# Optimization experiments

Hardware: AMD Instinct MI355X
Metric: run time of the kernel (lower is better)

Reference implementation:

```python
import jax, jax.numpy as jnp
import numpy as np
from jax import lax

V, E, HE, HD, B, T, DEC_STEPS = 50000, 300, 512, 1024, 64, 400, 80


def gru_cell(x, h, w_ih, w_hh, b_ih, b_hh):
    # PyTorch GRU cell semantics
    gi = x @ w_ih.T + b_ih          # [B, 3H]
    gh = h @ w_hh.T + b_hh          # [B, 3H]
    ir, iz, in_ = jnp.split(gi, 3, axis=-1)
    hr, hz, hn = jnp.split(gh, 3, axis=-1)
    r = jax.nn.sigmoid(ir + hr)
    z = jax.nn.sigmoid(iz + hz)
    n = jnp.tanh(in_ + r * hn)
    return (1.0 - z) * n + z * h


def setup_inputs() -> dict:
    key = jax.random.key(0)
    ks = jax.random.split(key, 20)
    s = 0.05
    texts = jax.random.randint(ks[0], (B, T), 0, V, dtype=jnp.int32)
    text_length = jax.random.randint(ks[1], (B,), 1, T + 1, dtype=jnp.int32)
    emb = jax.random.normal(ks[2], (V, E), jnp.float32) * s
    def w(k, shape):
        return jax.random.normal(k, shape, jnp.float32) * s
    return {
        "texts": texts,
        "text_length": text_length,
        "emb": emb,
        "enc_wih_f": w(ks[3], (3 * HE, E)),
        "enc_whh_f": w(ks[4], (3 * HE, HE)),
        "enc_bih_f": w(ks[5], (3 * HE,)),
        "enc_bhh_f": w(ks[6], (3 * HE,)),
        "enc_wih_b": w(ks[7], (3 * HE, E)),
        "enc_whh_b": w(ks[8], (3 * HE, HE)),
        "enc_bih_b": w(ks[9], (3 * HE,)),
        "enc_bhh_b": w(ks[10], (3 * HE,)),
        "dec_wih": w(ks[11], (3 * HD, E)),
        "dec_whh": w(ks[12], (3 * HD, HD)),
        "dec_bih": w(ks[13], (3 * HD,)),
        "dec_bhh": w(ks[14], (3 * HD,)),
        "out_w": w(ks[15], (V, HD)),
        "out_b": w(ks[16], (V,)),
    }


def reference(texts, text_length, emb,
              enc_wih_f, enc_whh_f, enc_bih_f, enc_bhh_f,
              enc_wih_b, enc_whh_b, enc_bih_b, enc_bhh_b,
              dec_wih, dec_whh, dec_bih, dec_bhh,
              out_w, out_b):
    b, t = texts.shape
    embed = emb[texts]                      # [B,T,E] (dropout is identity in eval)
    xs = jnp.swapaxes(embed, 0, 1)          # [T,B,E]
    lens = text_length[:, None]             # [B,1]
    h0 = jnp.zeros((b, HE), emb.dtype)

    # forward direction: final hidden = state at last valid timestep (pack semantics)
    def fstep(h, inp):
        x, tt = inp
        hn = gru_cell(x, h, enc_wih_f, enc_whh_f, enc_bih_f, enc_bhh_f)
        return jnp.where(tt < lens, hn, h), None
    hf, _ = lax.scan(fstep, h0, (xs, jnp.arange(t)))

    # backward direction: processes x[len-1] ... x[0]; skip padded positions
    def bstep(h, inp):
        x, tt = inp
        hn = gru_cell(x, h, enc_wih_b, enc_whh_b, enc_bih_b, enc_bhh_b)
        return jnp.where(tt < lens, hn, h), None
    hb, _ = lax.scan(bstep, h0, (xs[::-1], jnp.arange(t)[::-1]))

    hidden = jnp.concatenate([hf, hb], axis=-1)   # [B, 1024]

    sos = jnp.ones((b,), jnp.int32)               # inputs = ones
    def dstep(carry, _):
        h, tok = carry
        x = emb[tok]                              # [B,E]
        h = gru_cell(x, h, dec_wih, dec_whh, dec_bih, dec_bhh)
        logits = h @ out_w.T + out_b              # [B,V]
        tok = jnp.argmax(logits, axis=-1).astype(jnp.int32)
        return (h, tok), tok
    _, toks = lax.scan(dstep, (hidden, sos), None, length=DEC_STEPS)  # [80,B]

    return jnp.swapaxes(toks, 0, 1).astype(jnp.float32)[:, :, None]  # [B,80,1]
```

## Files before the change

### kernel.cpp

```cpp
#include <hip/hip_runtime.h>
#include <stdint.h>

typedef unsigned int u32;
typedef unsigned long long u64;
typedef unsigned short u16;
typedef __attribute__((ext_vector_type(8))) short s8;
typedef __attribute__((ext_vector_type(4))) float f4;

#define NWG 256
#define TPB 512
#define NB 64
#define TT 400
#define EE 300
#define HEN 512
#define HD 1024
#define VV 50000
#define DEC 80
#define NTL 3125
#define NTLP 3136
#define LCAP 512
#define PBOFF 131072
#define SMEMSZ (PBOFF + 16384)
#define RESC 0.00837f

#define BD_GRP   0
#define BD_ROOT  1024
#define BD_EPO   1152
#define BF_GRP   1280
#define BF_ROOT  2304
#define BF_EPO   2368
#define BX_GRP   2432
#define BX_ROOT  3456
#define BX_EPO   3520
#define BAR_WORDS 3584

struct P {
  const int* texts; const int* len; const float* emb;
  const float* ewih0; const float* ewhh0; const float* ebih0; const float* ebhh0;
  const float* ewih1; const float* ewhh1; const float* ebih1; const float* ebhh1;
  const float* dwih; const float* dwhh; const float* dbih; const float* dbhh;
  const float* outw; const float* outb;
  float* out;
  u16* owbf; float* xT; float* hTf; float* hTb; float* hTd; u16* hbf;
  u64* prt; int* tok; float* wn;
  u32* bar;
};

__device__ __forceinline__ float cld(const float* a) {
  return __hip_atomic_load(const_cast<float*>(a), __ATOMIC_RELAXED, __HIP_MEMORY_SCOPE_AGENT);
}
__device__ __forceinline__ void cst(float* a, float v) {
  __hip_atomic_store(a, v, __ATOMIC_RELAXED, __HIP_MEMORY_SCOPE_AGENT);
}
__device__ __forceinline__ u64 cld(const u64* a) {
  return __hip_atomic_load(const_cast<u64*>(a), __ATOMIC_RELAXED, __HIP_MEMORY_SCOPE_AGENT);
}
__device__ __forceinline__ void cst(u64* a, u64 v) {
  __hip_atomic_store(a, v, __ATOMIC_RELAXED, __HIP_MEMORY_SCOPE_AGENT);
}
__device__ __forceinline__ int cld(const int* a) {
  return __hip_atomic_load(const_cast<int*>(a), __ATOMIC_RELAXED, __HIP_MEMORY_SCOPE_AGENT);
}
__device__ __forceinline__ void cst(int* a, int v) {
  __hip_atomic_store(a, v, __ATOMIC_RELAXED, __HIP_MEMORY_SCOPE_AGENT);
}
__device__ __forceinline__ void cst(u16* a, u16 v) {
  __hip_atomic_store(a, v, __ATOMIC_RELAXED, __HIP_MEMORY_SCOPE_AGENT);
}

__device__ __forceinline__ void gbarx(u32* grp, u32* root, u32* epo,
                                      u32 e, u32 gsz, u32 nroot) {
  __syncthreads();
  if (threadIdx.x == 0) {
    u32 old = __hip_atomic_fetch_add(grp, 1u, __ATOMIC_RELAXED, __HIP_MEMORY_SCOPE_AGENT);
    if (old == e * gsz + (gsz - 1u)) {
      u32 r = __hip_atomic_fetch_add(root, 1u, __ATOMIC_RELAXED, __HIP_MEMORY_SCOPE_AGENT);
      if (r == e * nroot + (nroot - 1u))
        __hip_atomic_store(epo, e + 1u, __ATOMIC_RELAXED, __HIP_MEMORY_SCOPE_AGENT);
    }
    while (__hip_atomic_load(epo, __ATOMIC_RELAXED, __HIP_MEMORY_SCOPE_AGENT) < e + 1u)
      __builtin_amdgcn_s_sleep(8);
  }
  __syncthreads();
}

__device__ __forceinline__ u32 fkey(float v) {
  u32 u = __float_as_uint(v);
  return (u & 0x80000000u) ? ~u : (u | 0x80000000u);
}
__device__ __forceinline__ u16 f2bf(float f) {
  u32 u = __float_as_uint(f);
  u32 r = u + 0x7FFFu + ((u >> 16) & 1u);
  return (u16)(r >> 16);
}
__device__ __forceinline__ float sigm(float x) { return 1.f / (1.f + expf(-x)); }

__device__ __forceinline__ void gru_combine_epi(
    char* smem, const f4& ar, const f4& az, const f4& ax, const f4& ah,
    int jjb, int HL, const float* bih, const float* bhh,
    const float* hc, float* ho, int mask_t, const int* lenp, u16* hbf_out)
{
  const int tid = threadIdx.x, lane = tid & 63, wv = tid >> 6;
  float* pb = (float*)(smem + PBOFF);
  const int wl = wv & 3;
  if (wv < 4) {
    #pragma unroll
    for (int j = 0; j < 4; j++) {
      pb[((wl * 16 + j * 4 + 0) * 64) + lane] = ar[j];
      pb[((wl * 16 + j * 4 + 1) * 64) + lane] = az[j];
      pb[((wl * 16 + j * 4 + 2) * 64) + lane] = ax[j];
      pb[((wl * 16 + j * 4 + 3) * 64) + lane] = ah[j];
    }
  }
  __syncthreads();
  if (wv >= 4) {
    #pragma unroll
    for (int j = 0; j < 4; j++) {
      pb[((wl * 16 + j * 4 + 0) * 64) + lane] += ar[j];
      pb[((wl * 16 + j * 4 + 1) * 64) + lane] += az[j];
      pb[((wl * 16 + j * 4 + 2) * 64) + lane] += ax[j];
      pb[((wl * 16 + j * 4 + 3) * 64) + lane] += ah[j];
    }
  }
  __syncthreads();
  if (tid < 256) {
    int b = tid & 63, j = tid >> 6;
    int jj = jjb + j;
    float r = 0, z = 0, xn = 0, hn = 0;
    #pragma unroll
    for (int w = 0; w < 4; w++) {
      int base = ((w * 16 + j * 4) * 64) + b;
      r  += pb[base];
      z  += pb[base + 64];
      xn += pb[base + 128];
      hn += pb[base + 192];
    }
    r = sigm(r + bih[jj] + bhh[jj]);
    z = sigm(z + bih[HL + jj] + bhh[HL + jj]);
    float nn = tanhf(xn + bih[2 * HL + jj] + r * (hn + bhh[2 * HL + jj]));
    float hold = cld(hc + (size_t)jj * NB + b);
    float hv = (1.f - z) * nn + z * hold;
    if (lenp && mask_t >= lenp[b]) hv = hold;
    cst(ho + (size_t)jj * NB + b, hv);
    if (hbf_out) cst(hbf_out + (size_t)b * HD + jj, f2bf(hv));
  }
}

__device__ __forceinline__ void gru_enc(
    char* smem, int jjb, const float* xsrc,
    const float* bih, const float* bhh,
    const float* __restrict__ hc, float* ho, int tt, const int* lenp)
{
  const int tid = threadIdx.x, lane = tid & 63, wv = tid >> 6;
  const float* lw = (const float*)smem;
  const int KT = EE + HEN;
  const int vs = (wv * KT) >> 3, ve = ((wv + 1) * KT) >> 3;
  f4 ar = {0,0,0,0}, az = {0,0,0,0}, ax = {0,0,0,0}, ah = {0,0,0,0};
  const int xe = ve < EE ? ve : EE;
  int k = vs;
  for (; k + 8 <= xe; k += 8) {
    float xv[8];
    #pragma unroll
    for (int u = 0; u < 8; u++) xv[u] = xsrc[(size_t)(k + u) * NB + lane];
    #pragma unroll
    for (int u = 0; u < 8; u++) {
      const float* wp = lw + (k + u) * 12;
      f4 w0 = *(const f4*)wp; f4 w1 = *(const f4*)(wp + 4); f4 w2 = *(const f4*)(wp + 8);
      ar += xv[u] * w0; az += xv[u] * w1; ax += xv[u] * w2;
    }
  }
  for (; k < xe; k++) {
    float xv = xsrc[(size_t)k * NB + lane];
    const float* wp = lw + k * 12;
    f4 w0 = *(const f4*)wp; f4 w1 = *(const f4*)(wp + 4); f4 w2 = *(const f4*)(wp + 8);
    ar += xv * w0; az += xv * w1; ax += xv * w2;
  }
  k = vs > EE ? vs : EE;
  for (; k + 8 <= ve; k += 8) {
    float hv[8];
    #pragma unroll
    for (int u = 0; u < 8; u++) hv[u] = cld(hc + (size_t)(k + u - EE) * NB + lane);
    #pragma unroll
    for (int u = 0; u < 8; u++) {
      const float* wp = lw + (k + u) * 12;
      f4 w0 = *(const f4*)wp; f4 w1 = *(const f4*)(wp + 4); f4 w2 = *(const f4*)(wp + 8);
      ar += hv[u] * w0; az += hv[u] * w1; ah += hv[u] * w2;
    }
  }
  for (; k < ve; k++) {
    float hv = cld(hc + (size_t)(k - EE) * NB + lane);
    const float* wp = lw + k * 12;
    f4 w0 = *(const f4*)wp; f4 w1 = *(const f4*)(wp + 4); f4 w2 = *(const f4*)(wp + 8);
    ar += hv * w0; az += hv * w1; ah += hv * w2;
  }
  gru_combine_epi(smem, ar, az, ax, ah, jjb, HEN, bih, bhh, hc, ho, tt, lenp, nullptr);
}

__device__ __forceinline__ void gru_dec(
    const P& p, char* smem, int jjb,
    const float* __restrict__ hc, float* ho)
{
  const int tid = threadIdx.x, lane = tid & 63, wv = tid >> 6;
  const float* wih = p.dwih; const float* whh = p.dwhh;
  const int KT = EE + HD;
  const int vs = (wv * KT) >> 3, ve = ((wv + 1) * KT) >> 3;
  f4 ar = {0,0,0,0}, az = {0,0,0,0}, ax = {0,0,0,0}, ah = {0,0,0,0};
  const int xe = ve < EE ? ve : EE;
  if (vs < EE) {
    const float* xr = p.emb + (size_t)cld(p.tok + lane) * EE;
    int k = vs;
    for (; k + 4 <= xe; k += 4) {
      float xv[4];
      #pragma unroll
      for (int u = 0; u < 4; u++) xv[u] = xr[k + u];
      #pragma unroll
      for (int u = 0; u < 4; u++) {
        #pragma unroll
        for (int j = 0; j < 4; j++) {
          int jj = jjb + j;
          ar[j] = fmaf(xv[u], wih[(size_t)jj * EE + k + u], ar[j]);
          az[j] = fmaf(xv[u], wih[(size_t)(HD + jj) * EE + k + u], az[j]);
          ax[j] = fmaf(xv[u], wih[(size_t)(2 * HD + jj) * EE + k + u], ax[j]);
        }
      }
    }
    for (; k < xe; k++) {
      float xv = xr[k];
      #pragma unroll
      for (int j = 0; j < 4; j++) {
        int jj = jjb + j;
        ar[j] = fmaf(xv, wih[(size_t)jj * EE + k], ar[j]);
        az[j] = fmaf(xv, wih[(size_t)(HD + jj) * EE + k], az[j]);
        ax[j] = fmaf(xv, wih[(size_t)(2 * HD + jj) * EE + k], ax[j]);
      }
    }
  }
  int hs = vs - EE; if (hs < 0) hs = 0;
  const int he = ve - EE;
  int k = hs;
  for (; k + 4 <= he; k += 4) {
    float hv[4];
    #pragma unroll
    for (int u = 0; u < 4; u++) hv[u] = cld(hc + (size_t)(k + u) * NB + lane);
    #pragma unroll
    for (int u = 0; u < 4; u++) {
      #pragma unroll
      for (int j = 0; j < 4; j++) {
        int jj = jjb + j;
        ar[j] = fmaf(hv[u], whh[(size_t)jj * HD + k + u], ar[j]);
        az[j] = fmaf(hv[u], whh[(size_t)(HD + jj) * HD + k + u], az[j]);
        ah[j] = fmaf(hv[u], whh[(size_t)(2 * HD + jj) * HD + k + u], ah[j]);
      }
    }
  }
  for (; k < he; k++) {
    float hv = cld(hc + (size_t)k * NB + lane);
    #pragma unroll
    for (int j = 0; j < 4; j++) {
      int jj = jjb + j;
      ar[j] = fmaf(hv, whh[(size_t)jj * HD + k], ar[j]);
      az[j] = fmaf(hv, whh[(size_t)(HD + jj) * HD + k], az[j]);
      ah[j] = fmaf(hv, whh[(size_t)(2 * HD + jj) * HD + k], ah[j]);
    }
  }
  gru_combine_epi(smem, ar, az, ax, ah, jjb, HD, p.dbih, p.dbhh,
                  hc, ho, -1, nullptr, p.hbf);
}

__global__ void __launch_bounds__(TPB, 2) prep_kernel(P p) {
  const int wg = blockIdx.x, tid = threadIdx.x;
  const int lane = tid & 63, wv = tid >> 6;
  const int gtid = wg * TPB + tid;
  int gwv = wg * 8 + wv;
  for (int v = gwv; v < VV; v += 2048) {
    const float* wr = p.outw + (size_t)v * HD + lane * 16;
    u16* dst = p.owbf + (size_t)v * HD + lane * 16;
    float sa = 0.f;
    u32 pk[8];
    #pragma unroll
    for (int q = 0; q < 4; q++) {
      float4 f = *(const float4*)(wr + q * 4);
      sa += f.x * f.x + f.y * f.y + f.z * f.z + f.w * f.w;
      pk[q * 2 + 0] = (u32)f2bf(f.x) | ((u32)f2bf(f.y) << 16);
      pk[q * 2 + 1] = (u32)f2bf(f.z) | ((u32)f2bf(f.w) << 16);
    }
    *(uint4*)(dst)     = make_uint4(pk[0], pk[1], pk[2], pk[3]);
    *(uint4*)(dst + 8) = make_uint4(pk[4], pk[5], pk[6], pk[7]);
    #pragma unroll
    for (int d = 1; d < 64; d <<= 1) sa += __shfl_xor(sa, d);
    if (lane == 0) p.wn[v] = sqrtf(sa);
  }
  const long long tot = (long long)TT * NB * EE;
  for (long long i = gtid; i < tot; i += (long long)NWG * TPB) {
    int t = (int)(i / (NB * EE));
    int rr = (int)(i % (NB * EE));
    int b2 = rr / EE, k = rr % EE;
    float v = p.emb[(size_t)p.texts[b2 * TT + t] * EE + k];
    p.xT[((size_t)t * EE + k) * NB + b2] = v;
  }
}

__global__ void __launch_bounds__(TPB, 1) enc_kernel(P p) {
  extern __shared__ __align__(16) char smem[];
  const int wg = blockIdx.x, tid = threadIdx.x;
  const int lane = tid & 63, wv = tid >> 6;
  const int gtid = wg * TPB + tid;
  u32 ebD = 0, ebF = 0;
  const int dir = wg >> 7;
  const int ejjb = (wg & 127) * 4;

  {
    const float* wih = dir ? p.ewih1 : p.ewih0;
    const float* whh = dir ? p.ewhh1 : p.ewhh0;
    float* lw = (float*)smem;
    for (int c = wv; c < 12; c += 8) {
      int g = c >> 2, j = c & 3;
      const float* sx = wih + (size_t)(g * HEN + ejjb + j) * EE;
      for (int k = lane; k < EE; k += 64) lw[k * 12 + c] = sx[k];
      const float* sh = whh + (size_t)(g * HEN + ejjb + j) * HEN;
      for (int k = lane; k < HEN; k += 64) lw[(EE + k) * 12 + c] = sh[k];
    }
  }
  __syncthreads();

  {
    const float* bih = dir ? p.ebih1 : p.ebih0;
    const float* bhh = dir ? p.ebhh1 : p.ebhh0;
    float* hbase = dir ? p.hTb : p.hTf;
    for (int t = 0; t < TT; t++) {
      int te = dir ? (TT - 1 - t) : t;
      const float* hc = hbase + (size_t)(t & 1) * HEN * NB;
      float* ho = hbase + (size_t)((t + 1) & 1) * HEN * NB;
      gru_enc(smem, ejjb, p.xT + (size_t)te * EE * NB, bih, bhh, hc, ho, te, p.len);
      gbarx(p.bar + BD_GRP + ((wg >> 4) << 6),
            p.bar + BD_ROOT + dir * 64, p.bar + BD_EPO + dir * 64, ebD++, 16u, 8u);
    }
  }
  gbarx(p.bar + BF_GRP + ((wg >> 4) << 6),
        p.bar + BF_ROOT, p.bar + BF_EPO, ebF++, 16u, 16u);
  for (int i = gtid; i < HD * NB; i += NWG * TPB) {
    int k = i / NB, b2 = i % NB;
    float v = (k < HEN) ? cld(p.hTf + (size_t)k * NB + b2)
                        : cld(p.hTb + (size_t)(k - HEN) * NB + b2);
    cst(p.hTd + i, v);
  }
  if (gtid < NB) cst(p.tok + gtid, 1);
}

__global__ void __launch_bounds__(TPB, 1) dec_kernel(P p) {
  extern __shared__ __align__(16) char smem[];
  const int wg = blockIdx.x, tid = threadIdx.x;
  const int lane = tid & 63, wv = tid >> 6;
  u32 ebX = 0;

  for (int s = 0; s < DEC; s++) {
    const float* hc = p.hTd + (size_t)(s & 1) * HD * NB;
    float* ho = p.hTd + (size_t)((s + 1) & 1) * HD * NB;
    gru_dec(p, smem, wg * 4, hc, ho);
    gbarx(p.bar + BX_GRP + ((wg >> 4) << 6),
          p.bar + BX_ROOT, p.bar + BX_EPO, ebX++, 16u, 16u);
    {
      u16* hA = (u16*)smem;
      float* hsq = (float*)(smem + PBOFF);
      const int l15 = lane & 15, quad = lane >> 4;
      const int gw = wg * 8 + wv;
      const bool two = (gw + 2048) < NTL;
      if (tid < 64) hsq[tid] = 0.f;
      __syncthreads();
      const u64* hb64 = (const u64*)p.hbf;
      u64* hA64 = (u64*)hA;
      #pragma unroll 1
      for (int ii = 0; ii < 32; ii += 4) {
        u64 q[4];
        #pragma unroll
        for (int u = 0; u < 4; u++)
          q[u] = cld(hb64 + (size_t)(tid + (ii + u) * TPB));
        #pragma unroll
        for (int u = 0; u < 4; u++) {
          int i = tid + (ii + u) * TPB;
          int r = i >> 8, c = i & 255;
          int cc = c >> 1;
          hA64[(size_t)r * 256 + ((cc ^ (r & 7)) * 2) + (c & 1)] = q[u];
          u32 uu[2] = {(u32)q[u], (u32)(q[u] >> 32)};
          float sq = 0.f;
          #pragma unroll
          for (int t2 = 0; t2 < 2; t2++) {
            float lo = __uint_as_float(uu[t2] << 16);
            float hi = __uint_as_float(uu[t2] & 0xffff0000u);
            sq = fmaf(lo, lo, fmaf(hi, hi, sq));
          }
          atomicAdd(&hsq[r], sq);
        }
      }
      __syncthreads();
      f4 acc0[4], acc1[4];
      #pragma unroll
      for (int m = 0; m < 4; m++) {
        #pragma unroll
        for (int r = 0; r < 4; r++) { acc0[m][r] = 0.f; acc1[m][r] = 0.f; }
      }
      const u16* bp0 = p.owbf + (size_t)(gw * 16 + l15) * HD + quad * 8;
      const u16* bp1 = bp0 + (size_t)2048 * 16 * HD;
      const int x7 = l15 & 7;
      const u16* hrow = hA + l15 * 1024;
      #pragma unroll 4
      for (int kc = 0; kc < 32; kc++) {
        int ci = ((kc * 4 + quad) ^ x7) * 8;
        s8 b0 = *(const s8*)(bp0 + kc * 32);
        s8 a0 = *(const s8*)(hrow + ci);
        s8 a1 = *(const s8*)(hrow + 16384 + ci);
        s8 a2 = *(const s8*)(hrow + 32768 + ci);
        s8 a3 = *(const s8*)(hrow + 49152 + ci);
        acc0[0] = __builtin_amdgcn_mfma_f32_16x16x32_bf16(a0, b0, acc0[0], 0, 0, 0);
        acc0[1] = __builtin_amdgcn_mfma_f32_16x16x32_bf16(a1, b0, acc0[1], 0, 0, 0);
        acc0[2] = __builtin_amdgcn_mfma_f32_16x16x32_bf16(a2, b0, acc0[2], 0, 0, 0);
        acc0[3] = __builtin_amdgcn_mfma_f32_16x16x32_bf16(a3, b0, acc0[3], 0, 0, 0);
        if (two) {
          s8 b1 = *(const s8*)(bp1 + kc * 32);
          acc1[0] = __builtin_amdgcn_mfma_f32_16x16x32_bf16(a0, b1, acc1[0], 0, 0, 0);
          acc1[1] = __builtin_amdgcn_mfma_f32_16x16x32_bf16(a1, b1, acc1[1], 0, 0, 0);
          acc1[2] = __builtin_amdgcn_mfma_f32_16x16x32_bf16(a2, b1, acc1[2], 0, 0, 0);
          acc1[3] = __builtin_amdgcn_mfma_f32_16x16x32_bf16(a3, b1, acc1[3], 0, 0, 0);
        }
      }
      float hroot[4][4];
      #pragma unroll
      for (int m = 0; m < 4; m++)
        #pragma unroll
        for (int r = 0; r < 4; r++)
          hroot[m][r] = sqrtf(hsq[m * 16 + quad * 4 + r]);
      auto epi = [&](int nt, f4* acc) {
        int col = nt * 16 + l15;
        float bias = p.outb[col];
        float wnc = p.wn[col];
        #pragma unroll
        for (int m = 0; m < 4; m++) {
          #pragma unroll
          for (int r = 0; r < 4; r++) {
            float v = acc[m][r] + bias;
            float e = RESC * hroot[m][r] * wnc + 1e-5f;
            u32 klo = fkey(v - e), kup = fkey(v + e);
            #pragma unroll
            for (int d = 1; d < 16; d <<= 1) {
              u32 ol = __shfl_xor(klo, d); if (ol > klo) klo = ol;
              u32 ou = __shfl_xor(kup, d); if (ou > kup) kup = ou;
            }
            if (l15 == 0)
              cst(p.prt + (size_t)(m * 16 + quad * 4 + r) * NTLP + nt,
                  ((u64)klo << 32) | kup);
          }
        }
      };
      epi(gw, acc0);
      if (two) epi(gw + 2048, acc1);
    }
    gbarx(p.bar + BX_GRP + ((wg >> 4) << 6),
          p.bar + BX_ROOT, p.bar + BX_EPO, ebX++, 16u, 16u);
    if (wg < NB) {
      const int b = wg;
      char* ms = smem + PBOFF;
      float* hb = (float*)ms;
      u64* red = (u64*)(ms + 4096);
      u64* gmp = (u64*)(ms + 4160);
      u64* bestp = (u64*)(ms + 4168);
      int* ncp = (int*)(ms + 4176);
      int* list = (int*)(ms + 4192);
      for (int i = tid; i < HD; i += TPB) hb[i] = cld(ho + (size_t)i * NB + b);
      if (tid == 0) { *bestp = 0ull; *ncp = 0; }
      __syncthreads();
      u64 pv[7];
      u64 mx = 0;
      #pragma unroll
      for (int i = 0; i < 7; i++) {
        int nt = tid + i * TPB;
        pv[i] = (nt < NTL) ? cld(p.prt + (size_t)b * NTLP + nt) : 0ull;
        if (pv[i] > mx) mx = pv[i];
      }
      #pragma unroll
      for (int d = 1; d < 64; d <<= 1) { u64 o = __shfl_xor(mx, d); if (o > mx) mx = o; }
      if (lane == 0) red[wv] = mx;
      __syncthreads();
      if (tid == 0) {
        u64 g = red[0];
        for (int w2 = 1; w2 < 8; w2++) if (red[w2] > g) g = red[w2];
        *gmp = g;
      }
      __syncthreads();
      const u32 thr = (u32)(*gmp >> 32);
      #pragma unroll
      for (int i = 0; i < 7; i++) {
        if ((u32)pv[i] >= thr) {
          int ix = atomicAdd(ncp, 1);
          if (ix < LCAP) list[ix] = tid + i * TPB;
        }
      }
      __syncthreads();
      int total = *ncp;
      int nc = total < LCAP ? total : LCAP;
      const int c16 = tid >> 5, seg = tid & 31;
      u64 lb = 0;
      auto rescue = [&](int nt) {
        int v = nt * 16 + c16;
        const float* wr = p.outw + (size_t)v * HD;
        float sm = 0.f;
        #pragma unroll 8
        for (int i = 0; i < 32; i++) {
          int k = seg + 32 * i;
          sm = fmaf(hb[k], wr[k], sm);
        }
        #pragma unroll
        for (int d = 1; d < 32; d <<= 1) sm += __shfl_xor(sm, d);
        if (seg == 0) {
          float lg = sm + p.outb[v];
          u64 k2 = ((u64)fkey(lg) << 32) | (~(u32)v);
          if (k2 > lb) lb = k2;
        }
      };
      for (int ci = 0; ci < nc; ci++) rescue(list[ci]);
      if (total > LCAP) {
        for (int nt = 0; nt < NTL; nt++)
          if ((u32)cld(p.prt + (size_t)b * NTLP + nt) >= thr) rescue(nt);
      }
      if (seg == 0 && lb) atomicMax((unsigned long long*)bestp, lb);
      __syncthreads();
      if (tid == 0) {
        u32 v = ~(u32)(*bestp);
        cst(p.tok + b, (int)v);
        p.out[b * DEC + s] = (float)v;
      }
    }
    gbarx(p.bar + BX_GRP + ((wg >> 4) << 6),
          p.bar + BX_ROOT, p.bar + BX_EPO, ebX++, 16u, 16u);
  }
}

__global__ void seq2seq_init(u32* bar, float* hTf, float* hTb) {
  int g = blockIdx.x * blockDim.x + threadIdx.x;
  if (g < BAR_WORDS) bar[g] = 0u;
  int n = 2 * HEN * NB;
  for (int i = g; i < n; i += gridDim.x * blockDim.x) { hTf[i] = 0.f; hTb[i] = 0.f; }
}

extern "C" void kernel_launch(void* const* d_in, const int* in_sizes, int n_in,
                              void* d_out, int out_size, void* d_ws, size_t ws_size,
                              hipStream_t stream) {
  char* w = (char*)d_ws;
  size_t off = 0;
  auto carve = [&](size_t n) {
    void* q = w + off;
    off = (off + n + 255) & ~(size_t)255;
    return q;
  };
  P p;
  p.texts = (const int*)d_in[0];
  p.len   = (const int*)d_in[1];
  p.emb   = (const float*)d_in[2];
  p.ewih0 = (const float*)d_in[3];  p.ewhh0 = (const float*)d_in[4];
  p.ebih0 = (const float*)d_in[5];  p.ebhh0 = (const float*)d_in[6];
  p.ewih1 = (const float*)d_in[7];  p.ewhh1 = (const float*)d_in[8];
  p.ebih1 = (const float*)d_in[9];  p.ebhh1 = (const float*)d_in[10];
  p.dwih  = (const float*)d_in[11]; p.dwhh  = (const float*)d_in[12];
  p.dbih  = (const float*)d_in[13]; p.dbhh  = (const float*)d_in[14];
  p.outw  = (const float*)d_in[15]; p.outb  = (const float*)d_in[16];
  p.out   = (float*)d_out;
  p.owbf  = (u16*)carve((size_t)VV * HD * 2);
  p.xT    = (float*)carve((size_t)TT * EE * NB * 4);
  p.hTf   = (float*)carve((size_t)2 * HEN * NB * 4);
  p.hTb   = (float*)carve((size_t)2 * HEN * NB * 4);
  p.hTd   = (float*)carve((size_t)2 * HD * NB * 4);
  p.hbf   = (u16*)carve((size_t)NB * HD * 2);
  p.prt   = (u64*)carve((size_t)NB * NTLP * 8);
  p.tok   = (int*)carve(256);
  p.wn    = (float*)carve((size_t)VV * 4);
  p.bar   = (u32*)carve(BAR_WORDS * 4);
  if (off > ws_size) return;

  hipFuncSetAttribute((const void*)enc_kernel,
                      hipFuncAttributeMaxDynamicSharedMemorySize, SMEMSZ);
  hipFuncSetAttribute((const void*)dec_kernel,
                      hipFuncAttributeMaxDynamicSharedMemorySize, SMEMSZ);

  hipLaunchKernelGGL(seq2seq_init, dim3(64), dim3(256), 0, stream,
                     p.bar, p.hTf, p.hTb);
  hipLaunchKernelGGL(prep_kernel, dim3(NWG), dim3(TPB), 0, stream, p);
  void* args[] = { &p };
  hipError_t e = hipLaunchCooperativeKernel((void*)enc_kernel,
                                            dim3(NWG), dim3(TPB), args, SMEMSZ, stream);
  if (e != hipSuccess) {
    enc_kernel<<<dim3(NWG), dim3(TPB), SMEMSZ, stream>>>(p);
  }
  e = hipLaunchCooperativeKernel((void*)dec_kernel,
                                 dim3(NWG), dim3(TPB), args, SMEMSZ, stream);
  if (e != hipSuccess) {
    dec_kernel<<<dim3(NWG), dim3(TPB), SMEMSZ, stream>>>(p);
  }
}
```

Measured before the change: 17.98 ms.

## Replace persistent cooperative kernels with per-step kernel launches

Removes the persistent cooperative encoder and decoder kernels and their software grid barriers built on atomics. Each encoder timestep and each decoder stage (GRU, logits, rescue) becomes its own kernel launch, so kernel boundaries provide the synchronisation. This drops atomic loads and stores and barrier spinning. In exchange it adds about 640 launches, and every encoder launch reloads its weight slice into LDS.

```diff
diff --git a/kernel.cpp b/kernel.cpp
--- a/kernel.cpp
+++ b/kernel.cpp
@@ -19,20 +19,11 @@
 #define NTL 3125
 #define NTLP 3136
 #define LCAP 512
-#define PBOFF 131072
-#define SMEMSZ (PBOFF + 16384)
+#define EOFF 39168
+#define LGOFF 131072
+#define LGSZ (LGOFF + 256)
 #define RESC 0.00837f
 
-#define BD_GRP   0
-#define BD_ROOT  1024
-#define BD_EPO   1152
-#define BF_GRP   1280
-#define BF_ROOT  2304
-#define BF_EPO   2368
-#define BX_GRP   2432
-#define BX_ROOT  3456
-#define BX_EPO   3520
-#define BAR_WORDS 3584
 
 struct P {
   const int* texts; const int* len; const float* emb;
@@ -43,46 +34,7 @@
   float* out;
   u16* owbf; float* xT; float* hTf; float* hTb; float* hTd; u16* hbf;
   u64* prt; int* tok; float* wn;
-  u32* bar;
 };
-
-__device__ __forceinline__ float cld(const float* a) {
-  return __hip_atomic_load(const_cast<float*>(a), __ATOMIC_RELAXED, __HIP_MEMORY_SCOPE_AGENT);
-}
-__device__ __forceinline__ void cst(float* a, float v) {
-  __hip_atomic_store(a, v, __ATOMIC_RELAXED, __HIP_MEMORY_SCOPE_AGENT);
-}
-__device__ __forceinline__ u64 cld(const u64* a) {
-  return __hip_atomic_load(const_cast<u64*>(a), __ATOMIC_RELAXED, __HIP_MEMORY_SCOPE_AGENT);
-}
-__device__ __forceinline__ void cst(u64* a, u64 v) {
-  __hip_atomic_store(a, v, __ATOMIC_RELAXED, __HIP_MEMORY_SCOPE_AGENT);
-}
-__device__ __forceinline__ int cld(const int* a) {
-  return __hip_atomic_load(const_cast<int*>(a), __ATOMIC_RELAXED, __HIP_MEMORY_SCOPE_AGENT);
-}
-__device__ __forceinline__ void cst(int* a, int v) {
-  __hip_atomic_store(a, v, __ATOMIC_RELAXED, __HIP_MEMORY_SCOPE_AGENT);
-}
-__device__ __forceinline__ void cst(u16* a, u16 v) {
-  __hip_atomic_store(a, v, __ATOMIC_RELAXED, __HIP_MEMORY_SCOPE_AGENT);
-}
-
-__device__ __forceinline__ void gbarx(u32* grp, u32* root, u32* epo,
-                                      u32 e, u32 gsz, u32 nroot) {
-  __syncthreads();
-  if (threadIdx.x == 0) {
-    u32 old = __hip_atomic_fetch_add(grp, 1u, __ATOMIC_RELAXED, __HIP_MEMORY_SCOPE_AGENT);
-    if (old == e * gsz + (gsz - 1u)) {
-      u32 r = __hip_atomic_fetch_add(root, 1u, __ATOMIC_RELAXED, __HIP_MEMORY_SCOPE_AGENT);
-      if (r == e * nroot + (nroot - 1u))
-        __hip_atomic_store(epo, e + 1u, __ATOMIC_RELAXED, __HIP_MEMORY_SCOPE_AGENT);
-    }
-    while (__hip_atomic_load(epo, __ATOMIC_RELAXED, __HIP_MEMORY_SCOPE_AGENT) < e + 1u)
-      __builtin_amdgcn_s_sleep(8);
-  }
-  __syncthreads();
-}
 
 __device__ __forceinline__ u32 fkey(float v) {
   u32 u = __float_as_uint(v);
@@ -96,12 +48,11 @@
 __device__ __forceinline__ float sigm(float x) { return 1.f / (1.f + expf(-x)); }
 
 __device__ __forceinline__ void gru_combine_epi(
-    char* smem, const f4& ar, const f4& az, const f4& ax, const f4& ah,
+    float* pb, const f4& ar, const f4& az, const f4& ax, const f4& ah,
     int jjb, int HL, const float* bih, const float* bhh,
     const float* hc, float* ho, int mask_t, const int* lenp, u16* hbf_out)
 {
   const int tid = threadIdx.x, lane = tid & 63, wv = tid >> 6;
-  float* pb = (float*)(smem + PBOFF);
   const int wl = wv & 3;
   if (wv < 4) {
     #pragma unroll
@@ -138,20 +89,76 @@
     r = sigm(r + bih[jj] + bhh[jj]);
     z = sigm(z + bih[HL + jj] + bhh[HL + jj]);
     float nn = tanhf(xn + bih[2 * HL + jj] + r * (hn + bhh[2 * HL + jj]));
-    float hold = cld(hc + (size_t)jj * NB + b);
+    float hold = hc[(size_t)jj * NB + b];
     float hv = (1.f - z) * nn + z * hold;
     if (lenp && mask_t >= lenp[b]) hv = hold;
-    cst(ho + (size_t)jj * NB + b, hv);
-    if (hbf_out) cst(hbf_out + (size_t)b * HD + jj, f2bf(hv));
-  }
-}
-
-__device__ __forceinline__ void gru_enc(
-    char* smem, int jjb, const float* xsrc,
-    const float* bih, const float* bhh,
-    const float* __restrict__ hc, float* ho, int tt, const int* lenp)
-{
-  const int tid = threadIdx.x, lane = tid & 63, wv = tid >> 6;
+    ho[(size_t)jj * NB + b] = hv;
+    if (hbf_out) hbf_out[(size_t)b * HD + jj] = f2bf(hv);
+  }
+}
+
+__global__ void __launch_bounds__(TPB, 2) prep_kernel(P p) {
+  const int wg = blockIdx.x, tid = threadIdx.x;
+  const int lane = tid & 63, wv = tid >> 6;
+  const int gtid = wg * TPB + tid;
+  int gwv = wg * 8 + wv;
+  for (int v = gwv; v < VV; v += 2048) {
+    const float* wr = p.outw + (size_t)v * HD + lane * 16;
+    u16* dst = p.owbf + (size_t)v * HD + lane * 16;
+    float sa = 0.f;
+    u32 pk[8];
+    #pragma unroll
+    for (int q = 0; q < 4; q++) {
+      float4 f = *(const float4*)(wr + q * 4);
+      sa += f.x * f.x + f.y * f.y + f.z * f.z + f.w * f.w;
+      pk[q * 2 + 0] = (u32)f2bf(f.x) | ((u32)f2bf(f.y) << 16);
+      pk[q * 2 + 1] = (u32)f2bf(f.z) | ((u32)f2bf(f.w) << 16);
+    }
+    *(uint4*)(dst)     = make_uint4(pk[0], pk[1], pk[2], pk[3]);
+    *(uint4*)(dst + 8) = make_uint4(pk[4], pk[5], pk[6], pk[7]);
+    #pragma unroll
+    for (int d = 1; d < 64; d <<= 1) sa += __shfl_xor(sa, d);
+    if (lane == 0) p.wn[v] = sqrtf(sa);
+  }
+  const long long tot = (long long)TT * NB * EE;
+  for (long long i = gtid; i < tot; i += (long long)NWG * TPB) {
+    int t = (int)(i / (NB * EE));
+    int rr = (int)(i % (NB * EE));
+    int b2 = rr / EE, k = rr % EE;
+    float v = p.emb[(size_t)p.texts[b2 * TT + t] * EE + k];
+    p.xT[((size_t)t * EE + k) * NB + b2] = v;
+  }
+}
+
+__global__ void __launch_bounds__(TPB, 1) enc_step_kernel(P p, int t) {
+  __shared__ __align__(16) char smem[EOFF + 16384];
+  const int wg = blockIdx.x, tid = threadIdx.x;
+  const int lane = tid & 63, wv = tid >> 6;
+  const int dir = wg >> 7;
+  const int ejjb = (wg & 127) * 4;
+
+  {
+    const float* wih = dir ? p.ewih1 : p.ewih0;
+    const float* whh = dir ? p.ewhh1 : p.ewhh0;
+    float* lw = (float*)smem;
+    for (int c = wv; c < 12; c += 8) {
+      int g = c >> 2, j = c & 3;
+      const float* sx = wih + (size_t)(g * HEN + ejjb + j) * EE;
+      for (int k = lane; k < EE; k += 64) lw[k * 12 + c] = sx[k];
+      const float* sh = whh + (size_t)(g * HEN + ejjb + j) * HEN;
+      for (int k = lane; k < HEN; k += 64) lw[(EE + k) * 12 + c] = sh[k];
+    }
+  }
+  __syncthreads();
+
+  const float* bih = dir ? p.ebih1 : p.ebih0;
+  const float* bhh = dir ? p.ebhh1 : p.ebhh0;
+  float* hbase = dir ? p.hTb : p.hTf;
+  const int te = dir ? (TT - 1 - t) : t;
+  const float* hc = hbase + (size_t)(t & 1) * HEN * NB;
+  float* ho = hbase + (size_t)((t + 1) & 1) * HEN * NB;
+  const float* xsrc = p.xT + (size_t)te * EE * NB;
+
   const float* lw = (const float*)smem;
   const int KT = EE + HEN;
   const int vs = (wv * KT) >> 3, ve = ((wv + 1) * KT) >> 3;
@@ -179,7 +186,7 @@
   for (; k + 8 <= ve; k += 8) {
     float hv[8];
     #pragma unroll
-    for (int u = 0; u < 8; u++) hv[u] = cld(hc + (size_t)(k + u - EE) * NB + lane);
+    for (int u = 0; u < 8; u++) hv[u] = hc[(size_t)(k + u - EE) * NB + lane];
     #pragma unroll
     for (int u = 0; u < 8; u++) {
       const float* wp = lw + (k + u) * 12;
@@ -188,26 +195,41 @@
     }
   }
   for (; k < ve; k++) {
-    float hv = cld(hc + (size_t)(k - EE) * NB + lane);
+    float hv = hc[(size_t)(k - EE) * NB + lane];
     const float* wp = lw + k * 12;
     f4 w0 = *(const f4*)wp; f4 w1 = *(const f4*)(wp + 4); f4 w2 = *(const f4*)(wp + 8);
     ar += hv * w0; az += hv * w1; ah += hv * w2;
   }
-  gru_combine_epi(smem, ar, az, ax, ah, jjb, HEN, bih, bhh, hc, ho, tt, lenp, nullptr);
-}
-
-__device__ __forceinline__ void gru_dec(
-    const P& p, char* smem, int jjb,
-    const float* __restrict__ hc, float* ho)
-{
-  const int tid = threadIdx.x, lane = tid & 63, wv = tid >> 6;
+  gru_combine_epi((float*)(smem + EOFF), ar, az, ax, ah, ejjb, HEN,
+                  bih, bhh, hc, ho, te, p.len, nullptr);
+}
+
+__global__ void enc_join_kernel(P p) {
+  int g = blockIdx.x * blockDim.x + threadIdx.x;
+  int stride = gridDim.x * blockDim.x;
+  for (int i = g; i < HD * NB; i += stride) {
+    int k = i / NB, b2 = i % NB;
+    float v = (k < HEN) ? p.hTf[(size_t)k * NB + b2]
+                        : p.hTb[(size_t)(k - HEN) * NB + b2];
+    p.hTd[i] = v;
+  }
+  if (g < NB) p.tok[g] = 1;
+}
+
+__global__ void __launch_bounds__(TPB, 1) dec_gru_kernel(P p, int s) {
+  __shared__ __align__(16) float pb[4096];
+  const int wg = blockIdx.x, tid = threadIdx.x;
+  const int lane = tid & 63, wv = tid >> 6;
+  const int jjb = wg * 4;
+  const float* hc = p.hTd + (size_t)(s & 1) * HD * NB;
+  float* ho = p.hTd + (size_t)((s + 1) & 1) * HD * NB;
   const float* wih = p.dwih; const float* whh = p.dwhh;
   const int KT = EE + HD;
   const int vs = (wv * KT) >> 3, ve = ((wv + 1) * KT) >> 3;
   f4 ar = {0,0,0,0}, az = {0,0,0,0}, ax = {0,0,0,0}, ah = {0,0,0,0};
   const int xe = ve < EE ? ve : EE;
   if (vs < EE) {
-    const float* xr = p.emb + (size_t)cld(p.tok + lane) * EE;
+    const float* xr = p.emb + (size_t)p.tok[lane] * EE;
     int k = vs;
     for (; k + 4 <= xe; k += 4) {
       float xv[4];
@@ -241,7 +263,7 @@
   for (; k + 4 <= he; k += 4) {
     float hv[4];
     #pragma unroll
-    for (int u = 0; u < 4; u++) hv[u] = cld(hc + (size_t)(k + u) * NB + lane);
+    for (int u = 0; u < 4; u++) hv[u] = hc[(size_t)(k + u) * NB + lane];
     #pragma unroll
     for (int u = 0; u < 4; u++) {
       #pragma unroll
@@ -254,7 +276,7 @@
     }
   }
   for (; k < he; k++) {
-    float hv = cld(hc + (size_t)k * NB + lane);
+    float hv = hc[(size_t)k * NB + lane];
     #pragma unroll
     for (int j = 0; j < 4; j++) {
       int jj = jjb + j;
@@ -263,280 +285,174 @@
       ah[j] = fmaf(hv, whh[(size_t)(2 * HD + jj) * HD + k], ah[j]);
     }
   }
-  gru_combine_epi(smem, ar, az, ax, ah, jjb, HD, p.dbih, p.dbhh,
+  gru_combine_epi(pb, ar, az, ax, ah, jjb, HD, p.dbih, p.dbhh,
                   hc, ho, -1, nullptr, p.hbf);
 }
 
-__global__ void __launch_bounds__(TPB, 2) prep_kernel(P p) {
-  const int wg = blockIdx.x, tid = threadIdx.x;
-  const int lane = tid & 63, wv = tid >> 6;
-  const int gtid = wg * TPB + tid;
-  int gwv = wg * 8 + wv;
-  for (int v = gwv; v < VV; v += 2048) {
-    const float* wr = p.outw + (size_t)v * HD + lane * 16;
-    u16* dst = p.owbf + (size_t)v * HD + lane * 16;
-    float sa = 0.f;
-    u32 pk[8];
-    #pragma unroll
-    for (int q = 0; q < 4; q++) {
-      float4 f = *(const float4*)(wr + q * 4);
-      sa += f.x * f.x + f.y * f.y + f.z * f.z + f.w * f.w;
-      pk[q * 2 + 0] = (u32)f2bf(f.x) | ((u32)f2bf(f.y) << 16);
-      pk[q * 2 + 1] = (u32)f2bf(f.z) | ((u32)f2bf(f.w) << 16);
-    }
-    *(uint4*)(dst)     = make_uint4(pk[0], pk[1], pk[2], pk[3]);
-    *(uint4*)(dst + 8) = make_uint4(pk[4], pk[5], pk[6], pk[7]);
-    #pragma unroll
-    for (int d = 1; d < 64; d <<= 1) sa += __shfl_xor(sa, d);
-    if (lane == 0) p.wn[v] = sqrtf(sa);
-  }
-  const long long tot = (long long)TT * NB * EE;
-  for (long long i = gtid; i < tot; i += (long long)NWG * TPB) {
-    int t = (int)(i / (NB * EE));
-    int rr = (int)(i % (NB * EE));
-    int b2 = rr / EE, k = rr % EE;
-    float v = p.emb[(size_t)p.texts[b2 * TT + t] * EE + k];
-    p.xT[((size_t)t * EE + k) * NB + b2] = v;
-  }
-}
-
-__global__ void __launch_bounds__(TPB, 1) enc_kernel(P p) {
+__global__ void __launch_bounds__(TPB, 1) dec_logits_kernel(P p) {
   extern __shared__ __align__(16) char smem[];
   const int wg = blockIdx.x, tid = threadIdx.x;
   const int lane = tid & 63, wv = tid >> 6;
-  const int gtid = wg * TPB + tid;
-  u32 ebD = 0, ebF = 0;
-  const int dir = wg >> 7;
-  const int ejjb = (wg & 127) * 4;
-
-  {
-    const float* wih = dir ? p.ewih1 : p.ewih0;
-    const float* whh = dir ? p.ewhh1 : p.ewhh0;
-    float* lw = (float*)smem;
-    for (int c = wv; c < 12; c += 8) {
-      int g = c >> 2, j = c & 3;
-      const float* sx = wih + (size_t)(g * HEN + ejjb + j) * EE;
-      for (int k = lane; k < EE; k += 64) lw[k * 12 + c] = sx[k];
-      const float* sh = whh + (size_t)(g * HEN + ejjb + j) * HEN;
-      for (int k = lane; k < HEN; k += 64) lw[(EE + k) * 12 + c] = sh[k];
-    }
-  }
-  __syncthreads();
-
-  {
-    const float* bih = dir ? p.ebih1 : p.ebih0;
-    const float* bhh = dir ? p.ebhh1 : p.ebhh0;
-    float* hbase = dir ? p.hTb : p.hTf;
-    for (int t = 0; t < TT; t++) {
-      int te = dir ? (TT - 1 - t) : t;
-      const float* hc = hbase + (size_t)(t & 1) * HEN * NB;
-      float* ho = hbase + (size_t)((t + 1) & 1) * HEN * NB;
-      gru_enc(smem, ejjb, p.xT + (size_t)te * EE * NB, bih, bhh, hc, ho, te, p.len);
-      gbarx(p.bar + BD_GRP + ((wg >> 4) << 6),
-            p.bar + BD_ROOT + dir * 64, p.bar + BD_EPO + dir * 64, ebD++, 16u, 8u);
-    }
-  }
-  gbarx(p.bar + BF_GRP + ((wg >> 4) << 6),
-        p.bar + BF_ROOT, p.bar + BF_EPO, ebF++, 16u, 16u);
-  for (int i = gtid; i < HD * NB; i += NWG * TPB) {
-    int k = i / NB, b2 = i % NB;
-    float v = (k < HEN) ? cld(p.hTf + (size_t)k * NB + b2)
-                        : cld(p.hTb + (size_t)(k - HEN) * NB + b2);
-    cst(p.hTd + i, v);
-  }
-  if (gtid < NB) cst(p.tok + gtid, 1);
-}
-
-__global__ void __launch_bounds__(TPB, 1) dec_kernel(P p) {
-  extern __shared__ __align__(16) char smem[];
-  const int wg = blockIdx.x, tid = threadIdx.x;
+  u16* hA = (u16*)smem;
+  float* hsq = (float*)(smem + LGOFF);
+  const int l15 = lane & 15, quad = lane >> 4;
+  const int gw = wg * 8 + wv;
+  const bool two = (gw + 2048) < NTL;
+  if (tid < 64) hsq[tid] = 0.f;
+  __syncthreads();
+  for (int i = tid; i < 8192; i += TPB) {
+    int r = i >> 7, c = i & 127;
+    uint4 q = *(const uint4*)(p.hbf + (size_t)r * HD + c * 8);
+    *(uint4*)(hA + (size_t)r * 1024 + ((c ^ (r & 7)) * 8)) = q;
+    u32 uu[4] = {q.x, q.y, q.z, q.w};
+    float sq = 0.f;
+    #pragma unroll
+    for (int t2 = 0; t2 < 4; t2++) {
+      float lo = __uint_as_float(uu[t2] << 16);
+      float hi = __uint_as_float(uu[t2] & 0xffff0000u);
+      sq = fmaf(lo, lo, fmaf(hi, hi, sq));
+    }
+    atomicAdd(&hsq[r], sq);
+  }
+  __syncthreads();
+  f4 acc0[4], acc1[4];
+  #pragma unroll
+  for (int m = 0; m < 4; m++) {
+    #pragma unroll
+    for (int r = 0; r < 4; r++) { acc0[m][r] = 0.f; acc1[m][r] = 0.f; }
+  }
+  const u16* bp0 = p.owbf + (size_t)(gw * 16 + l15) * HD + quad * 8;
+  const u16* bp1 = bp0 + (size_t)2048 * 16 * HD;
+  const int x7 = l15 & 7;
+  const u16* hrow = hA + l15 * 1024;
+  #pragma unroll 4
+  for (int kc = 0; kc < 32; kc++) {
+    int ci = ((kc * 4 + quad) ^ x7) * 8;
+    s8 b0 = *(const s8*)(bp0 + kc * 32);
+    s8 a0 = *(const s8*)(hrow + ci);
+    s8 a1 = *(const s8*)(hrow + 16384 + ci);
+    s8 a2 = *(const s8*)(hrow + 32768 + ci);
+    s8 a3 = *(const s8*)(hrow + 49152 + ci);
+    acc0[0] = __builtin_amdgcn_mfma_f32_16x16x32_bf16(a0, b0, acc0[0], 0, 0, 0);
+    acc0[1] = __builtin_amdgcn_mfma_f32_16x16x32_bf16(a1, b0, acc0[1], 0, 0, 0);
+    acc0[2] = __builtin_amdgcn_mfma_f32_16x16x32_bf16(a2, b0, acc0[2], 0, 0, 0);
+    acc0[3] = __builtin_amdgcn_mfma_f32_16x16x32_bf16(a3, b0, acc0[3], 0, 0, 0);
+    if (two) {
+      s8 b1 = *(const s8*)(bp1 + kc * 32);
+      acc1[0] = __builtin_amdgcn_mfma_f32_16x16x32_bf16(a0, b1, acc1[0], 0, 0, 0);
+      acc1[1] = __builtin_amdgcn_mfma_f32_16x16x32_bf16(a1, b1, acc1[1], 0, 0, 0);
+      acc1[2] = __builtin_amdgcn_mfma_f32_16x16x32_bf16(a2, b1, acc1[2], 0, 0, 0);
+      acc1[3] = __builtin_amdgcn_mfma_f32_16x16x32_bf16(a3, b1, acc1[3], 0, 0, 0);
+    }
+  }
+  float hroot[4][4];
+  #pragma unroll
+  for (int m = 0; m < 4; m++)
+    #pragma unroll
+    for (int r = 0; r < 4; r++)
+      hroot[m][r] = sqrtf(hsq[m * 16 + quad * 4 + r]);
+  auto epi = [&](int nt, f4* acc) {
+    int col = nt * 16 + l15;
+    float bias = p.outb[col];
+    float wnc = p.wn[col];
+    #pragma unroll
+    for (int m = 0; m < 4; m++) {
+      #pragma unroll
+      for (int r = 0; r < 4; r++) {
+        float v = acc[m][r] + bias;
+        float e = RESC * hroot[m][r] * wnc + 1e-5f;
+        u32 klo = fkey(v - e), kup = fkey(v + e);
+        #pragma unroll
+        for (int d = 1; d < 16; d <<= 1) {
+          u32 ol = __shfl_xor(klo, d); if (ol > klo) klo = ol;
+          u32 ou = __shfl_xor(kup, d); if (ou > kup) kup = ou;
+        }
+        if (l15 == 0)
+          p.prt[(size_t)(m * 16 + quad * 4 + r) * NTLP + nt] =
+              ((u64)klo << 32) | kup;
+      }
+    }
+  };
+  epi(gw, acc0);
+  if (two) epi(gw + 2048, acc1);
+}
+
+__global__ void __launch_bounds__(TPB, 1) dec_rescue_kernel(P p, int s) {
+  __shared__ float hb[HD];
+  __shared__ u64 red[8];
+  __shared__ u64 gmp, bestp;
+  __shared__ int ncp;
+  __shared__ int list[LCAP];
+  const int b = blockIdx.x, tid = threadIdx.x;
   const int lane = tid & 63, wv = tid >> 6;
-  u32 ebX = 0;
-
-  for (int s = 0; s < DEC; s++) {
-    const float* hc = p.hTd + (size_t)(s & 1) * HD * NB;
-    float* ho = p.hTd + (size_t)((s + 1) & 1) * HD * NB;
-    gru_dec(p, smem, wg * 4, hc, ho);
-    gbarx(p.bar + BX_GRP + ((wg >> 4) << 6),
-          p.bar + BX_ROOT, p.bar + BX_EPO, ebX++, 16u, 16u);
-    {
-      u16* hA = (u16*)smem;
-      float* hsq = (float*)(smem + PBOFF);
-      const int l15 = lane & 15, quad = lane >> 4;
-      const int gw = wg * 8 + wv;
-      const bool two = (gw + 2048) < NTL;
-      if (tid < 64) hsq[tid] = 0.f;
-      __syncthreads();
-      const u64* hb64 = (const u64*)p.hbf;
-      u64* hA64 = (u64*)hA;
-      #pragma unroll 1
-      for (int ii = 0; ii < 32; ii += 4) {
-        u64 q[4];
-        #pragma unroll
-        for (int u = 0; u < 4; u++)
-          q[u] = cld(hb64 + (size_t)(tid + (ii + u) * TPB));
-        #pragma unroll
-        for (int u = 0; u < 4; u++) {
-          int i = tid + (ii + u) * TPB;
-          int r = i >> 8, c = i & 255;
-          int cc = c >> 1;
-          hA64[(size_t)r * 256 + ((cc ^ (r & 7)) * 2) + (c & 1)] = q[u];
-          u32 uu[2] = {(u32)q[u], (u32)(q[u] >> 32)};
-          float sq = 0.f;
-          #pragma unroll
-          for (int t2 = 0; t2 < 2; t2++) {
-            float lo = __uint_as_float(uu[t2] << 16);
-            float hi = __uint_as_float(uu[t2] & 0xffff0000u);
-            sq = fmaf(lo, lo, fmaf(hi, hi, sq));
-          }
-          atomicAdd(&hsq[r], sq);
-        }
-      }
-      __syncthreads();
-      f4 acc0[4], acc1[4];
-      #pragma unroll
-      for (int m = 0; m < 4; m++) {
-        #pragma unroll
-        for (int r = 0; r < 4; r++) { acc0[m][r] = 0.f; acc1[m][r] = 0.f; }
-      }
-      const u16* bp0 = p.owbf + (size_t)(gw * 16 + l15) * HD + quad * 8;
-      const u16* bp1 = bp0 + (size_t)2048 * 16 * HD;
-      const int x7 = l15 & 7;
-      const u16* hrow = hA + l15 * 1024;
-      #pragma unroll 4
-      for (int kc = 0; kc < 32; kc++) {
-        int ci = ((kc * 4 + quad) ^ x7) * 8;
-        s8 b0 = *(const s8*)(bp0 + kc * 32);
-        s8 a0 = *(const s8*)(hrow + ci);
-        s8 a1 = *(const s8*)(hrow + 16384 + ci);
-        s8 a2 = *(const s8*)(hrow + 32768 + ci);
-        s8 a3 = *(const s8*)(hrow + 49152 + ci);
-        acc0[0] = __builtin_amdgcn_mfma_f32_16x16x32_bf16(a0, b0, acc0[0], 0, 0, 0);
-        acc0[1] = __builtin_amdgcn_mfma_f32_16x16x32_bf16(a1, b0, acc0[1], 0, 0, 0);
-        acc0[2] = __builtin_amdgcn_mfma_f32_16x16x32_bf16(a2, b0, acc0[2], 0, 0, 0);
-        acc0[3] = __builtin_amdgcn_mfma_f32_16x16x32_bf16(a3, b0, acc0[3], 0, 0, 0);
-        if (two) {
-          s8 b1 = *(const s8*)(bp1 + kc * 32);
-          acc1[0] = __builtin_amdgcn_mfma_f32_16x16x32_bf16(a0, b1, acc1[0], 0, 0, 0);
-          acc1[1] = __builtin_amdgcn_mfma_f32_16x16x32_bf16(a1, b1, acc1[1], 0, 0, 0);
-          acc1[2] = __builtin_amdgcn_mfma_f32_16x16x32_bf16(a2, b1, acc1[2], 0, 0, 0);
-          acc1[3] = __builtin_amdgcn_mfma_f32_16x16x32_bf16(a3, b1, acc1[3], 0, 0, 0);
-        }
-      }
-      float hroot[4][4];
-      #pragma unroll
-      for (int m = 0; m < 4; m++)
-        #pragma unroll
-        for (int r = 0; r < 4; r++)
-          hroot[m][r] = sqrtf(hsq[m * 16 + quad * 4 + r]);
-      auto epi = [&](int nt, f4* acc) {
-        int col = nt * 16 + l15;
-        float bias = p.outb[col];
-        float wnc = p.wn[col];
-        #pragma unroll
-        for (int m = 0; m < 4; m++) {
-          #pragma unroll
-          for (int r = 0; r < 4; r++) {
-            float v = acc[m][r] + bias;
-            float e = RESC * hroot[m][r] * wnc + 1e-5f;
-            u32 klo = fkey(v - e), kup = fkey(v + e);
-            #pragma unroll
-            for (int d = 1; d < 16; d <<= 1) {
-              u32 ol = __shfl_xor(klo, d); if (ol > klo) klo = ol;
-              u32 ou = __shfl_xor(kup, d); if (ou > kup) kup = ou;
-            }
-            if (l15 == 0)
-              cst(p.prt + (size_t)(m * 16 + quad * 4 + r) * NTLP + nt,
-                  ((u64)klo << 32) | kup);
-          }
-        }
-      };
-      epi(gw, acc0);
-      if (two) epi(gw + 2048, acc1);
-    }
-    gbarx(p.bar + BX_GRP + ((wg >> 4) << 6),
-          p.bar + BX_ROOT, p.bar + BX_EPO, ebX++, 16u, 16u);
-    if (wg < NB) {
-      const int b = wg;
-      char* ms = smem + PBOFF;
-      float* hb = (float*)ms;
-      u64* red = (u64*)(ms + 4096);
-      u64* gmp = (u64*)(ms + 4160);
-      u64* bestp = (u64*)(ms + 4168);
-      int* ncp = (int*)(ms + 4176);
-      int* list = (int*)(ms + 4192);
-      for (int i = tid; i < HD; i += TPB) hb[i] = cld(ho + (size_t)i * NB + b);
-      if (tid == 0) { *bestp = 0ull; *ncp = 0; }
-      __syncthreads();
-      u64 pv[7];
-      u64 mx = 0;
-      #pragma unroll
-      for (int i = 0; i < 7; i++) {
-        int nt = tid + i * TPB;
-        pv[i] = (nt < NTL) ? cld(p.prt + (size_t)b * NTLP + nt) : 0ull;
-        if (pv[i] > mx) mx = pv[i];
-      }
-      #pragma unroll
-      for (int d = 1; d < 64; d <<= 1) { u64 o = __shfl_xor(mx, d); if (o > mx) mx = o; }
-      if (lane == 0) red[wv] = mx;
-      __syncthreads();
-      if (tid == 0) {
-        u64 g = red[0];
-        for (int w2 = 1; w2 < 8; w2++) if (red[w2] > g) g = red[w2];
-        *gmp = g;
-      }
-      __syncthreads();
-      const u32 thr = (u32)(*gmp >> 32);
-      #pragma unroll
-      for (int i = 0; i < 7; i++) {
-        if ((u32)pv[i] >= thr) {
-          int ix = atomicAdd(ncp, 1);
-          if (ix < LCAP) list[ix] = tid + i * TPB;
-        }
-      }
-      __syncthreads();
-      int total = *ncp;
-      int nc = total < LCAP ? total : LCAP;
-      const int c16 = tid >> 5, seg = tid & 31;
-      u64 lb = 0;
-      auto rescue = [&](int nt) {
-        int v = nt * 16 + c16;
-        const float* wr = p.outw + (size_t)v * HD;
-        float sm = 0.f;
-        #pragma unroll 8
-        for (int i = 0; i < 32; i++) {
-          int k = seg + 32 * i;
-          sm = fmaf(hb[k], wr[k], sm);
-        }
-        #pragma unroll
-        for (int d = 1; d < 32; d <<= 1) sm += __shfl_xor(sm, d);
-        if (seg == 0) {
-          float lg = sm + p.outb[v];
-          u64 k2 = ((u64)fkey(lg) << 32) | (~(u32)v);
-          if (k2 > lb) lb = k2;
-        }
-      };
-      for (int ci = 0; ci < nc; ci++) rescue(list[ci]);
-      if (total > LCAP) {
-        for (int nt = 0; nt < NTL; nt++)
-          if ((u32)cld(p.prt + (size_t)b * NTLP + nt) >= thr) rescue(nt);
-      }
-      if (seg == 0 && lb) atomicMax((unsigned long long*)bestp, lb);
-      __syncthreads();
-      if (tid == 0) {
-        u32 v = ~(u32)(*bestp);
-        cst(p.tok + b, (int)v);
-        p.out[b * DEC + s] = (float)v;
-      }
-    }
-    gbarx(p.bar + BX_GRP + ((wg >> 4) << 6),
-          p.bar + BX_ROOT, p.bar + BX_EPO, ebX++, 16u, 16u);
-  }
-}
-
-__global__ void seq2seq_init(u32* bar, float* hTf, float* hTb) {
+  const float* ho = p.hTd + (size_t)((s + 1) & 1) * HD * NB;
+  for (int i = tid; i < HD; i += TPB) hb[i] = ho[(size_t)i * NB + b];
+  if (tid == 0) { bestp = 0ull; ncp = 0; }
+  __syncthreads();
+  u64 pv[7];
+  u64 mx = 0;
+  #pragma unroll
+  for (int i = 0; i < 7; i++) {
+    int nt = tid + i * TPB;
+    pv[i] = (nt < NTL) ? p.prt[(size_t)b * NTLP + nt] : 0ull;
+    if (pv[i] > mx) mx = pv[i];
+  }
+  #pragma unroll
+  for (int d = 1; d < 64; d <<= 1) { u64 o = __shfl_xor(mx, d); if (o > mx) mx = o; }
+  if (lane == 0) red[wv] = mx;
+  __syncthreads();
+  if (tid == 0) {
+    u64 g = red[0];
+    for (int w2 = 1; w2 < 8; w2++) if (red[w2] > g) g = red[w2];
+    gmp = g;
+  }
+  __syncthreads();
+  const u32 thr = (u32)(gmp >> 32);
+  #pragma unroll
+  for (int i = 0; i < 7; i++) {
+    if ((u32)pv[i] >= thr) {
+      int ix = atomicAdd(&ncp, 1);
+      if (ix < LCAP) list[ix] = tid + i * TPB;
+    }
+  }
+  __syncthreads();
+  int total = ncp;
+  int nc = total < LCAP ? total : LCAP;
+  const int c16 = tid >> 5, seg = tid & 31;
+  u64 lb = 0;
+  auto rescue = [&](int nt) {
+    int v = nt * 16 + c16;
+    const float* wr = p.outw + (size_t)v * HD;
+    float sm = 0.f;
+    #pragma unroll 8
+    for (int i = 0; i < 32; i++) {
+      int k = seg + 32 * i;
+      sm = fmaf(hb[k], wr[k], sm);
+    }
+    #pragma unroll
+    for (int d = 1; d < 32; d <<= 1) sm += __shfl_xor(sm, d);
+    if (seg == 0) {
+      float lg = sm + p.outb[v];
+      u64 k2 = ((u64)fkey(lg) << 32) | (~(u32)v);
+      if (k2 > lb) lb = k2;
+    }
+  };
+  for (int ci = 0; ci < nc; ci++) rescue(list[ci]);
+  if (total > LCAP) {
+    for (int nt = 0; nt < NTL; nt++)
+      if ((u32)p.prt[(size_t)b * NTLP + nt] >= thr) rescue(nt);
+  }
+  if (seg == 0 && lb) atomicMax((unsigned long long*)&bestp, lb);
+  __syncthreads();
+  if (tid == 0) {
+    u32 v = ~(u32)(bestp);
+    p.tok[b] = (int)v;
+    p.out[b * DEC + s] = (float)v;
+  }
+}
+
+__global__ void seq2seq_init(float* hTf, float* hTb) {
   int g = blockIdx.x * blockDim.x + threadIdx.x;
-  if (g < BAR_WORDS) bar[g] = 0u;
   int n = 2 * HEN * NB;
   for (int i = g; i < n; i += gridDim.x * blockDim.x) { hTf[i] = 0.f; hTb[i] = 0.f; }
 }
@@ -572,26 +488,19 @@
   p.prt   = (u64*)carve((size_t)NB * NTLP * 8);
   p.tok   = (int*)carve(256);
   p.wn    = (float*)carve((size_t)VV * 4);
-  p.bar   = (u32*)carve(BAR_WORDS * 4);
   if (off > ws_size) return;
 
-  hipFuncSetAttribute((const void*)enc_kernel,
-                      hipFuncAttributeMaxDynamicSharedMemorySize, SMEMSZ);
-  hipFuncSetAttribute((const void*)dec_kernel,
-                      hipFuncAttributeMaxDynamicSharedMemorySize, SMEMSZ);
-
-  hipLaunchKernelGGL(seq2seq_init, dim3(64), dim3(256), 0, stream,
-                     p.bar, p.hTf, p.hTb);
-  hipLaunchKernelGGL(prep_kernel, dim3(NWG), dim3(TPB), 0, stream, p);
-  void* args[] = { &p };
-  hipError_t e = hipLaunchCooperativeKernel((void*)enc_kernel,
-                                            dim3(NWG), dim3(TPB), args, SMEMSZ, stream);
-  if (e != hipSuccess) {
-    enc_kernel<<<dim3(NWG), dim3(TPB), SMEMSZ, stream>>>(p);
-  }
-  e = hipLaunchCooperativeKernel((void*)dec_kernel,
-                                 dim3(NWG), dim3(TPB), args, SMEMSZ, stream);
-  if (e != hipSuccess) {
-    dec_kernel<<<dim3(NWG), dim3(TPB), SMEMSZ, stream>>>(p);
-  }
-}
+  hipFuncSetAttribute((const void*)dec_logits_kernel,
+                      hipFuncAttributeMaxDynamicSharedMemorySize, LGSZ);
+
+  seq2seq_init<<<dim3(64), dim3(256), 0, stream>>>(p.hTf, p.hTb);
+  prep_kernel<<<dim3(NWG), dim3(TPB), 0, stream>>>(p);
+  for (int t = 0; t < TT; t++)
+    enc_step_kernel<<<dim3(NWG), dim3(TPB), 0, stream>>>(p, t);
+  enc_join_kernel<<<dim3(64), dim3(256), 0, stream>>>(p);
+  for (int s = 0; s < DEC; s++) {
+    dec_gru_kernel<<<dim3(NWG), dim3(TPB), 0, stream>>>(p, s);
+    dec_logits_kernel<<<dim3(NWG), dim3(TPB), LGSZ, stream>>>(p);
+    dec_rescue_kernel<<<dim3(NB), dim3(TPB), 0, stream>>>(p, s);
+  }
+}
```

Result: faster. 14.70 ms (-18.3%).
